# Kernel tuning notes

Measured on AMD Instinct MI355X. Metric: run time of the kernel, lower is better.

## Reference

```python
import jax, jax.numpy as jnp
import numpy as np

NUM_SCALE_LAYERS = [16, 8, 8]
B, H, N = 32, 512, 64
NUM_PROPS = 2080


def _pool_specs():
    # (kernel, stride) per layer, matching the torch ModuleList construction
    specs = []
    for scale_idx, num_layer in enumerate(NUM_SCALE_LAYERS):
        first = (1, 1) if scale_idx == 0 else (3, 2)
        specs.append([first] + [(2, 1)] * (num_layer - 1))
    return specs


def _maxpool1d(x, k, s):
    # x: [B, H, L] -> valid max pool along last axis
    return jax.lax.reduce_window(x, -jnp.inf, jax.lax.max,
                                 (1, 1, k), (1, 1, s), 'VALID')


def setup_inputs() -> dict:
    key = jax.random.key(0)
    kx, ks, ke = jax.random.split(key, 3)
    x = jax.random.normal(kx, (B, H, N), dtype=jnp.float32)
    starts = jax.random.randint(ks, (NUM_PROPS,), 0, N)          # props[:,0] in [0, N)
    ends = jax.random.randint(ke, (NUM_PROPS,), 1, N + 1)        # props[:,1] in [1, N]
    props = jnp.stack([starts, ends], axis=1).astype(jnp.int64)
    return {"x": x, "props": props}


def reference(x, props):
    batch_size, hidden_size, ori_num_clips = x.shape
    ori_map_h = jnp.zeros((batch_size, hidden_size, ori_num_clips, ori_num_clips), x.dtype)
    ori_map_mask = jnp.zeros((batch_size, 1, ori_num_clips, ori_num_clips), x.dtype)
    acum_layers = 0
    stride = 1
    for scale_layers in _pool_specs():
        for i, (k, s) in enumerate(scale_layers):
            stride = stride * s
            x = _maxpool1d(x, k, s)
            # static (trace-time) diagonal index lists, exactly as the torch code
            s_idxs = np.arange(0, ori_num_clips - acum_layers - i * stride, stride)
            e_idxs = s_idxs + acum_layers + i * stride
            ori_map_h = ori_map_h.at[:, :, s_idxs, e_idxs].set(x)
            ori_map_mask = ori_map_mask.at[:, :, s_idxs, e_idxs].set(1.0)
        acum_layers += stride * (len(scale_layers) + 1)
    props_h = ori_map_h[:, :, props[:, 0], props[:, 1] - 1]      # [B, H, P]
    ori_map_mask = ori_map_mask.at[:, :, props[:, 0], props[:, 1] - 1].set(1.0)
    return props_h.swapaxes(1, 2), ori_map_h, ori_map_mask
```

## Files before the change

### kernel.cpp

```cpp
#include <hip/hip_runtime.h>
#include <math.h>

#define PB 32
#define PH 512
#define PN 64
#define PP 2080

#define OFF_MAP  ((size_t)PB * PP * PH)
#define OFF_MASK (OFF_MAP + (size_t)PB * PH * PN * PN)

__device__ __forceinline__ bool pair_valid(int s, int e) {
    int d = e - s;
    if (d < 0) return false;
    if (d <= 15) return true;
    if (d <= 31) return (d & 1) && !(s & 1);
    return d >= 35 && ((d & 3) == 3) && !(s & 3);
}

#define K1_ROWS 8
#define K1_RS 392
#define K1_ZERO 390

__global__ __launch_bounds__(256) void map_kernel(const float* __restrict__ x,
                                                  float* __restrict__ out) {
    __shared__ float L[K1_ROWS * K1_RS];
    const int tid  = threadIdx.x;
    const int wave = tid >> 6;
    const int lane = tid & 63;

    int a1[16], a2[16];
#pragma unroll
    for (int i = 0; i < 16; ++i) {
        const int s = wave * 16 + i;
        const int e = lane;
        const bool good = pair_valid(s, e);
        const int k = good ? min(31 - __clz(e - s + 1), 5) : 0;
        a1[i] = good ? 65 * k + s : K1_ZERO;
        a2[i] = good ? 65 * k + (e + 1 - (1 << k)) : K1_ZERO;
    }

    const size_t rowBase = (size_t)blockIdx.x * K1_ROWS;
#pragma unroll
    for (int i = tid; i < K1_ROWS * 64; i += 256) {
        const int r = i >> 6, c = i & 63;
        L[r * K1_RS + c] = x[rowBase * 64 + i];
    }
    if (tid < K1_ROWS) L[tid * K1_RS + K1_ZERO] = 0.0f;
    __syncthreads();

#pragma unroll
    for (int k = 1; k <= 5; ++k) {
        const int off = 1 << (k - 1);
#pragma unroll
        for (int i = tid; i < K1_ROWS * 64; i += 256) {
            const int r = i >> 6, c = i & 63;
            const float* Lp = L + r * K1_RS + 65 * (k - 1);
            L[r * K1_RS + 65 * k + c] = fmaxf(Lp[c], Lp[min(c + off, 63)]);
        }
        __syncthreads();
    }

#pragma unroll 2
    for (int r = 0; r < K1_ROWS; ++r) {
        const float* Lr = L + r * K1_RS;
        float* orow = out + OFF_MAP + (rowBase + r) * 4096 + lane;
#pragma unroll
        for (int i = 0; i < 16; ++i) {
            orow[(wave * 16 + i) * 64] = fmaxf(Lr[a1[i]], Lr[a2[i]]);
        }
    }
}

#define K2_LVL 2112
#define K2_ZROW (6 * K2_LVL)
#define K2_PA 12706

__global__ __launch_bounds__(256) void props_kernel(const float* __restrict__ x,
                                                    const int* __restrict__ props,
                                                    float* __restrict__ out) {
    __shared__ float Lf[K2_PA + 2 * PP];
    int* Li = (int*)Lf;

    const int tid = threadIdx.x;
    const int b  = blockIdx.y;
    const int h0 = blockIdx.x * 32;

    const float* xb = x + ((size_t)b * PH + h0) * PN;
#pragma unroll
    for (int i = tid; i < 32 * 64; i += 256) {
        const int h = i >> 6, n = i & 63;
        Lf[n * 33 + h] = xb[i];
    }
    if (tid < 33) Lf[K2_ZROW + tid] = 0.0f;

    for (int p = tid; p < PP; p += 256) {
        const int2 pr = ((const int2*)props)[p];
        const int s  = pr.x;
        const int e1 = pr.y - 1;
        const bool good = pair_valid(s, e1);
        const int k = good ? min(31 - __clz(e1 - s + 1), 5) : 0;
        Li[K2_PA + 2 * p]     = good ? k * K2_LVL + s * 33 : K2_ZROW;
        Li[K2_PA + 2 * p + 1] = good ? k * K2_LVL + (e1 + 1 - (1 << k)) * 33 : K2_ZROW;
    }
    __syncthreads();

#pragma unroll 1
    for (int k = 1; k <= 5; ++k) {
        const int off = 1 << (k - 1);
#pragma unroll
        for (int i = tid; i < 64 * 32; i += 256) {
            const int n = i >> 5, h = i & 31;
            const float* Lp = Lf + (k - 1) * K2_LVL;
            Lf[k * K2_LVL + n * 33 + h] = fmaxf(Lp[n * 33 + h], Lp[min(n + off, 63) * 33 + h]);
        }
        __syncthreads();
    }

    const int wave = tid >> 6;
    const int sub  = (tid >> 5) & 1;
    const int h    = tid & 31;
    float* ob = out + (size_t)b * PP * PH + h0 + h;
#pragma unroll 4
    for (int i = 0; i < PP / 8; ++i) {
        const int idx = i * 8 + wave * 2 + sub;
        const int2 aa = *(const int2*)&Li[K2_PA + 2 * idx];
        const float v = fmaxf(Lf[aa.x + h], Lf[aa.y + h]);
        ob[(size_t)idx * PH] = v;
    }
}

__global__ void mask_base_kernel(float* __restrict__ out) {
    const int gid = blockIdx.x * blockDim.x + threadIdx.x;
    const int l4 = (gid & 1023) * 4;
    float4 v;
    float* vv = (float*)&v;
#pragma unroll
    for (int q = 0; q < 4; ++q) {
        const int lin = l4 + q;
        vv[q] = pair_valid(lin >> 6, lin & 63) ? 1.0f : 0.0f;
    }
    ((float4*)(out + OFF_MASK))[gid] = v;
}

__global__ void mask_props_kernel(const int* __restrict__ props,
                                  float* __restrict__ out) {
    const int idx = blockIdx.x * blockDim.x + threadIdx.x;
    if (idx >= PB * PP) return;
    const int b = idx / PP;
    const int p = idx - b * PP;
    const int s  = props[2 * p];
    const int e1 = props[2 * p + 1] - 1;
    out[OFF_MASK + (size_t)b * (PN * PN) + s * PN + e1] = 1.0f;
}

extern "C" void kernel_launch(void* const* d_in, const int* in_sizes, int n_in,
                              void* d_out, int out_size, void* d_ws, size_t ws_size,
                              hipStream_t stream) {
    const float* x = (const float*)d_in[0];
    const int* props = (const int*)d_in[1];
    float* out = (float*)d_out;

    map_kernel<<<(PB * PH) / K1_ROWS, 256, 0, stream>>>(x, out);

    dim3 g2(PH / 32, PB);
    props_kernel<<<g2, 256, 0, stream>>>(x, props, out);

    mask_base_kernel<<<(PB * 1024) / 256, 256, 0, stream>>>(out);
    mask_props_kernel<<<(PB * PP + 255) / 256, 256, 0, stream>>>(props, out);
}
```

Measured before the change: 411.7 us.

## Fuse map, props, and mask kernels into one interleaved launch

Merges the four kernels into a single launch whose blocks are role-split: four map blocks for every props block, interleaved so both kinds of work run concurrently, plus 32 mask blocks. Each mask block builds the per-batch mask in LDS, applies the props, then writes it with float4 stores. This removes the separate mask_props scatter and the extra launches. The props path now recomputes the gather indices per element instead of staging them in LDS, which cuts LDS use and adds some ALU work.

```diff
diff --git a/kernel.cpp b/kernel.cpp
--- a/kernel.cpp
+++ b/kernel.cpp
@@ -17,140 +17,134 @@
     return d >= 35 && ((d & 3) == 3) && !(s & 3);
 }
 
+#define K2_LVL 2112
+#define K2_ZROW 12672
+#define LDS_FLOATS 12706
+
 #define K1_ROWS 8
 #define K1_RS 392
 #define K1_ZERO 390
 
-__global__ __launch_bounds__(256) void map_kernel(const float* __restrict__ x,
-                                                  float* __restrict__ out) {
-    __shared__ float L[K1_ROWS * K1_RS];
-    const int tid  = threadIdx.x;
-    const int wave = tid >> 6;
-    const int lane = tid & 63;
+#define GRID_BLOCKS 2592
 
-    int a1[16], a2[16];
+__global__ __launch_bounds__(256) void fused_kernel(const float* __restrict__ x,
+                                                    const int* __restrict__ props,
+                                                    float* __restrict__ out) {
+    __shared__ float Lf[LDS_FLOATS];
+    const int tid = threadIdx.x;
+    const int g = blockIdx.x;
+
+    if (g < 2560) {
+        const int q = g / 5;
+        const int r = g - q * 5;
+        if (r != 0) {
+            const int kb = q * 4 + (r - 1);
+            const size_t rowBase = (size_t)kb * K1_ROWS;
+            const int wave = tid >> 6;
+            const int lane = tid & 63;
+
+            int a1[16], a2[16];
 #pragma unroll
-    for (int i = 0; i < 16; ++i) {
-        const int s = wave * 16 + i;
-        const int e = lane;
-        const bool good = pair_valid(s, e);
-        const int k = good ? min(31 - __clz(e - s + 1), 5) : 0;
-        a1[i] = good ? 65 * k + s : K1_ZERO;
-        a2[i] = good ? 65 * k + (e + 1 - (1 << k)) : K1_ZERO;
-    }
-
-    const size_t rowBase = (size_t)blockIdx.x * K1_ROWS;
-#pragma unroll
-    for (int i = tid; i < K1_ROWS * 64; i += 256) {
-        const int r = i >> 6, c = i & 63;
-        L[r * K1_RS + c] = x[rowBase * 64 + i];
-    }
-    if (tid < K1_ROWS) L[tid * K1_RS + K1_ZERO] = 0.0f;
-    __syncthreads();
+            for (int i = 0; i < 16; ++i) {
+                const int s = wave * 16 + i;
+                const int e = lane;
+                const bool good = pair_valid(s, e);
+                const int k = good ? min(31 - __clz(e - s + 1), 5) : 0;
+                a1[i] = good ? 65 * k + s : K1_ZERO;
+                a2[i] = good ? 65 * k + (e + 1 - (1 << k)) : K1_ZERO;
+            }
 
 #pragma unroll
-    for (int k = 1; k <= 5; ++k) {
-        const int off = 1 << (k - 1);
+            for (int i = tid; i < K1_ROWS * 64; i += 256) {
+                const int rr = i >> 6, c = i & 63;
+                Lf[rr * K1_RS + c] = x[rowBase * 64 + i];
+            }
+            if (tid < K1_ROWS) Lf[tid * K1_RS + K1_ZERO] = 0.0f;
+            __syncthreads();
+
 #pragma unroll
-        for (int i = tid; i < K1_ROWS * 64; i += 256) {
-            const int r = i >> 6, c = i & 63;
-            const float* Lp = L + r * K1_RS + 65 * (k - 1);
-            L[r * K1_RS + 65 * k + c] = fmaxf(Lp[c], Lp[min(c + off, 63)]);
+            for (int k = 1; k <= 5; ++k) {
+                const int off = 1 << (k - 1);
+#pragma unroll
+                for (int i = tid; i < K1_ROWS * 64; i += 256) {
+                    const int rr = i >> 6, c = i & 63;
+                    const float* Lp = Lf + rr * K1_RS + 65 * (k - 1);
+                    Lf[rr * K1_RS + 65 * k + c] = fmaxf(Lp[c], Lp[min(c + off, 63)]);
+                }
+                __syncthreads();
+            }
+
+#pragma unroll 2
+            for (int rr = 0; rr < K1_ROWS; ++rr) {
+                const float* Lr = Lf + rr * K1_RS;
+                float* orow = out + OFF_MAP + (rowBase + rr) * 4096 + lane;
+#pragma unroll
+                for (int i = 0; i < 16; ++i) {
+                    orow[(wave * 16 + i) * 64] = fmaxf(Lr[a1[i]], Lr[a2[i]]);
+                }
+            }
+        } else {
+            const int b  = q >> 4;
+            const int h0 = (q & 15) * 32;
+
+            const float* xb = x + ((size_t)b * PH + h0) * PN;
+#pragma unroll
+            for (int i = tid; i < 32 * 64; i += 256) {
+                const int h = i >> 6, n = i & 63;
+                Lf[n * 33 + h] = xb[i];
+            }
+            if (tid < 33) Lf[K2_ZROW + tid] = 0.0f;
+            __syncthreads();
+
+#pragma unroll 1
+            for (int k = 1; k <= 5; ++k) {
+                const int off = 1 << (k - 1);
+#pragma unroll
+                for (int i = tid; i < 64 * 32; i += 256) {
+                    const int n = i >> 5, h = i & 31;
+                    const float* Lp = Lf + (k - 1) * K2_LVL;
+                    Lf[k * K2_LVL + n * 33 + h] =
+                        fmaxf(Lp[n * 33 + h], Lp[min(n + off, 63) * 33 + h]);
+                }
+                __syncthreads();
+            }
+
+            const int wave = tid >> 6;
+            const int sub  = (tid >> 5) & 1;
+            const int h    = tid & 31;
+            const int2* props2 = (const int2*)props;
+            float* ob = out + (size_t)b * PP * PH + h0 + h;
+#pragma unroll 4
+            for (int i = 0; i < PP / 8; ++i) {
+                const int idx = i * 8 + wave * 2 + sub;
+                const int2 pr = props2[idx];
+                const int s = pr.x, e1 = pr.y - 1;
+                const bool good = pair_valid(s, e1);
+                const int k = good ? min(31 - __clz(e1 - s + 1), 5) : 0;
+                const int A1 = good ? k * K2_LVL + s * 33 : K2_ZROW;
+                const int A2 = good ? k * K2_LVL + (e1 + 1 - (1 << k)) * 33 : K2_ZROW;
+                ob[(size_t)idx * PH] = fmaxf(Lf[A1 + h], Lf[A2 + h]);
+            }
+        }
+    } else {
+        const int b = g - 2560;
+
+        for (int i = tid; i < 4096; i += 256)
+            Lf[i] = pair_valid(i >> 6, i & 63) ? 1.0f : 0.0f;
+        __syncthreads();
+
+        for (int p = tid; p < PP; p += 256) {
+            const int2 pr = ((const int2*)props)[p];
+            Lf[pr.x * 64 + (pr.y - 1)] = 1.0f;
         }
         __syncthreads();
+
+        float4* ob = (float4*)(out + OFF_MASK + (size_t)b * 4096);
+        const float4* lb = (const float4*)Lf;
+#pragma unroll
+        for (int i = tid; i < 1024; i += 256)
+            ob[i] = lb[i];
     }
-
-#pragma unroll 2
-    for (int r = 0; r < K1_ROWS; ++r) {
-        const float* Lr = L + r * K1_RS;
-        float* orow = out + OFF_MAP + (rowBase + r) * 4096 + lane;
-#pragma unroll
-        for (int i = 0; i < 16; ++i) {
-            orow[(wave * 16 + i) * 64] = fmaxf(Lr[a1[i]], Lr[a2[i]]);
-        }
-    }
-}
-
-#define K2_LVL 2112
-#define K2_ZROW (6 * K2_LVL)
-#define K2_PA 12706
-
-__global__ __launch_bounds__(256) void props_kernel(const float* __restrict__ x,
-                                                    const int* __restrict__ props,
-                                                    float* __restrict__ out) {
-    __shared__ float Lf[K2_PA + 2 * PP];
-    int* Li = (int*)Lf;
-
-    const int tid = threadIdx.x;
-    const int b  = blockIdx.y;
-    const int h0 = blockIdx.x * 32;
-
-    const float* xb = x + ((size_t)b * PH + h0) * PN;
-#pragma unroll
-    for (int i = tid; i < 32 * 64; i += 256) {
-        const int h = i >> 6, n = i & 63;
-        Lf[n * 33 + h] = xb[i];
-    }
-    if (tid < 33) Lf[K2_ZROW + tid] = 0.0f;
-
-    for (int p = tid; p < PP; p += 256) {
-        const int2 pr = ((const int2*)props)[p];
-        const int s  = pr.x;
-        const int e1 = pr.y - 1;
-        const bool good = pair_valid(s, e1);
-        const int k = good ? min(31 - __clz(e1 - s + 1), 5) : 0;
-        Li[K2_PA + 2 * p]     = good ? k * K2_LVL + s * 33 : K2_ZROW;
-        Li[K2_PA + 2 * p + 1] = good ? k * K2_LVL + (e1 + 1 - (1 << k)) * 33 : K2_ZROW;
-    }
-    __syncthreads();
-
-#pragma unroll 1
-    for (int k = 1; k <= 5; ++k) {
-        const int off = 1 << (k - 1);
-#pragma unroll
-        for (int i = tid; i < 64 * 32; i += 256) {
-            const int n = i >> 5, h = i & 31;
-            const float* Lp = Lf + (k - 1) * K2_LVL;
-            Lf[k * K2_LVL + n * 33 + h] = fmaxf(Lp[n * 33 + h], Lp[min(n + off, 63) * 33 + h]);
-        }
-        __syncthreads();
-    }
-
-    const int wave = tid >> 6;
-    const int sub  = (tid >> 5) & 1;
-    const int h    = tid & 31;
-    float* ob = out + (size_t)b * PP * PH + h0 + h;
-#pragma unroll 4
-    for (int i = 0; i < PP / 8; ++i) {
-        const int idx = i * 8 + wave * 2 + sub;
-        const int2 aa = *(const int2*)&Li[K2_PA + 2 * idx];
-        const float v = fmaxf(Lf[aa.x + h], Lf[aa.y + h]);
-        ob[(size_t)idx * PH] = v;
-    }
-}
-
-__global__ void mask_base_kernel(float* __restrict__ out) {
-    const int gid = blockIdx.x * blockDim.x + threadIdx.x;
-    const int l4 = (gid & 1023) * 4;
-    float4 v;
-    float* vv = (float*)&v;
-#pragma unroll
-    for (int q = 0; q < 4; ++q) {
-        const int lin = l4 + q;
-        vv[q] = pair_valid(lin >> 6, lin & 63) ? 1.0f : 0.0f;
-    }
-    ((float4*)(out + OFF_MASK))[gid] = v;
-}
-
-__global__ void mask_props_kernel(const int* __restrict__ props,
-                                  float* __restrict__ out) {
-    const int idx = blockIdx.x * blockDim.x + threadIdx.x;
-    if (idx >= PB * PP) return;
-    const int b = idx / PP;
-    const int p = idx - b * PP;
-    const int s  = props[2 * p];
-    const int e1 = props[2 * p + 1] - 1;
-    out[OFF_MASK + (size_t)b * (PN * PN) + s * PN + e1] = 1.0f;
 }
 
 extern "C" void kernel_launch(void* const* d_in, const int* in_sizes, int n_in,
@@ -160,11 +154,5 @@
     const int* props = (const int*)d_in[1];
     float* out = (float*)d_out;
 
-    map_kernel<<<(PB * PH) / K1_ROWS, 256, 0, stream>>>(x, out);
-
-    dim3 g2(PH / 32, PB);
-    props_kernel<<<g2, 256, 0, stream>>>(x, props, out);
-
-    mask_base_kernel<<<(PB * 1024) / 256, 256, 0, stream>>>(out);
-    mask_props_kernel<<<(PB * PP + 255) / 256, 256, 0, stream>>>(props, out);
+    fused_kernel<<<GRID_BLOCKS, 256, 0, stream>>>(x, props, out);
 }
```

Result: slower. 440.1 us (+6.9%).
